# Kernel tuning notes

Hardware: AMD Instinct MI355X
Metric: run time of the kernel (lower is better)

## Reference

```python
import jax, jax.numpy as jnp
import numpy as np
import math

D_MODEL = 1024
N_HEADS = 16
D_HEAD = D_MODEL // N_HEADS


def setup_inputs() -> dict:
    key = jax.random.key(0)
    ks = jax.random.split(key, 5)
    B, T, C = 4, 2048, D_MODEL
    s = 1.0 / math.sqrt(C)
    return {
        "x": jax.random.normal(ks[0], (B, T, C), dtype=jnp.float32),
        "qkv_w": jax.random.normal(ks[1], (3 * C, C), dtype=jnp.float32) * s,
        "qkv_b": jnp.zeros((3 * C,), dtype=jnp.float32),
        "out_w": jax.random.normal(ks[2], (C, C), dtype=jnp.float32) * s,
        "out_b": jnp.zeros((C,), dtype=jnp.float32),
    }


def reference(x, qkv_w, qkv_b, out_w, out_b):
    B, T, C = x.shape
    H, Dh = N_HEADS, D_HEAD
    qkv = x @ qkv_w.T + qkv_b              # [B,T,3C] (torch Linear: x W^T + b)
    q, k, v = jnp.split(qkv, 3, axis=-1)
    # [B,T,C] -> [B,H,T,Dh]
    q = q.reshape(B, T, H, Dh).transpose(0, 2, 1, 3)
    k = k.reshape(B, T, H, Dh).transpose(0, 2, 1, 3)
    v = v.reshape(B, T, H, Dh).transpose(0, 2, 1, 3)
    att = jnp.einsum("bhqd,bhkd->bhqk", q, k) / math.sqrt(Dh)
    causal = jnp.tril(jnp.ones((T, T), dtype=bool))  # True = keep
    att = jnp.where(causal, att, -jnp.inf)
    att = jax.nn.softmax(att, axis=-1)
    y = jnp.einsum("bhqk,bhkd->bhqd", att, v)
    y = y.transpose(0, 2, 1, 3).reshape(B, T, C)
    return y @ out_w.T + out_b
```

## Files before the change

### kernel.cpp

```cpp
#include <hip/hip_runtime.h>

typedef __attribute__((ext_vector_type(4))) float f32x4;
typedef __attribute__((ext_vector_type(16))) float f32x16;
typedef __attribute__((ext_vector_type(8))) __bf16 bf16x8;
typedef __attribute__((ext_vector_type(4))) __bf16 bf16x4;
typedef __attribute__((ext_vector_type(2))) unsigned u32x2;

#define MFMA_B16(a,b,c) __builtin_amdgcn_mfma_f32_16x16x32_bf16((a),(b),(c),0,0,0)
#define MFMA32(a,b,c)  __builtin_amdgcn_mfma_f32_32x32x16_bf16((a),(b),(c),0,0,0)

static constexpr int T_LEN  = 2048;
static constexpr int C_DIM  = 1024;
static constexpr int H_NUM  = 16;
static constexpr int D_HEADc = 64;
static constexpr float Q_PRESCALE = 0.125f * 1.4426950408889634f;

__device__ __forceinline__ void async16(const void* g, void* l) {
  __builtin_amdgcn_global_load_lds(
      (const __attribute__((address_space(1))) unsigned int*)g,
      (__attribute__((address_space(3))) unsigned int*)l, 16, 0, 0);
}

__device__ __forceinline__ unsigned cvtpk(float lo, float hi) {
  unsigned r;
  asm("v_cvt_pk_bf16_f32 %0, %1, %2" : "=v"(r) : "v"(lo), "v"(hi));
  return r;
}

__global__ __launch_bounds__(256) void cvt3_kernel(const float* __restrict__ a, __bf16* __restrict__ da, int na,
                                                   const float* __restrict__ b, __bf16* __restrict__ db, int nb,
                                                   const float* __restrict__ c, __bf16* __restrict__ dc, int nc) {
  int i = blockIdx.x * 256 + threadIdx.x;
  const float* s;
  __bf16* d;
  long j;
  if (i < na) { s = a; d = da; j = i; }
  else if (i < na + nb) { s = b; d = db; j = i - na; }
  else if (i < na + nb + nc) { s = c; d = dc; j = i - na - nb; }
  else return;
  float4 f = reinterpret_cast<const float4*>(s)[j];
  bf16x4 o;
  o.x = (__bf16)f.x; o.y = (__bf16)f.y; o.z = (__bf16)f.z; o.w = (__bf16)f.w;
  reinterpret_cast<bf16x4*>(d)[j] = o;
}

__global__ __launch_bounds__(512, 2) void gemm_qkv(const __bf16* __restrict__ A,
                                                   const __bf16* __restrict__ W,
                                                   const float* __restrict__ bias,
                                                   __bf16* __restrict__ qb,
                                                   __bf16* __restrict__ kb,
                                                   __bf16* __restrict__ vb) {
  constexpr int K = 1024;
  __shared__ __bf16 As[2][128 * 64];
  __shared__ __bf16 Bs[2][128 * 64];
  const int tid = threadIdx.x;
  const int wid = tid >> 6, lane = tid & 63, l16 = lane & 15, lg = lane >> 4;
  const int r8 = lane >> 3, sl = lane & 7;
  const int r7 = l16 & 7;
  const int wm = wid >> 2, wn = wid & 3;
  const int m0 = blockIdx.x * 128;
  const int n0 = blockIdx.y * 128;

  f32x4 acc[4][2];
#pragma unroll
  for (int i = 0; i < 4; ++i)
#pragma unroll
    for (int j = 0; j < 2; ++j) acc[i][j] = f32x4{0.f, 0.f, 0.f, 0.f};

  auto stageg = [&](int buf, int k0) {
#pragma unroll
    for (int it = 0; it < 2; ++it) {
      int chunk = it * 8 + wid;
      int row = chunk * 8 + r8;
      int scol = ((sl ^ (row & 7)) << 3);
      async16(A + (long)(m0 + row) * K + k0 + scol, &As[buf][chunk * 512]);
      async16(W + (long)(n0 + row) * K + k0 + scol, &Bs[buf][chunk * 512]);
    }
  };

  stageg(0, 0);
  int cur = 0;
  for (int k0 = 0; k0 < K; k0 += 64) {
    if (k0 + 64 < K) {
      stageg(cur ^ 1, k0 + 64);
      asm volatile("s_waitcnt vmcnt(4)" ::: "memory");
    } else {
      asm volatile("s_waitcnt vmcnt(0)" ::: "memory");
    }
    __builtin_amdgcn_s_barrier();
#pragma unroll
    for (int kt = 0; kt < 2; ++kt) {
      const int sw = ((((kt << 2) | lg) ^ r7) << 3);
      bf16x8 af[4], bfv[2];
#pragma unroll
      for (int mi = 0; mi < 4; ++mi)
        af[mi] = *reinterpret_cast<const bf16x8*>(&As[cur][(wm * 64 + mi * 16 + l16) * 64 + sw]);
#pragma unroll
      for (int nt = 0; nt < 2; ++nt)
        bfv[nt] = *reinterpret_cast<const bf16x8*>(&Bs[cur][(wn * 32 + nt * 16 + l16) * 64 + sw]);
#pragma unroll
      for (int mi = 0; mi < 4; ++mi)
#pragma unroll
        for (int nt = 0; nt < 2; ++nt)
          acc[mi][nt] = MFMA_B16(af[mi], bfv[nt], acc[mi][nt]);
    }
    __builtin_amdgcn_s_barrier();
    cur ^= 1;
  }

  const int which = n0 >> 10;
  if (which == 0) {
#pragma unroll
    for (int mi = 0; mi < 4; ++mi)
#pragma unroll
      for (int nt = 0; nt < 2; ++nt)
#pragma unroll
        for (int r = 0; r < 4; ++r) {
          int m = m0 + wm * 64 + mi * 16 + lg * 4 + r;
          int n = n0 + wn * 32 + nt * 16 + l16;
          int cc = n & 1023;
          int h = cc >> 6, d = cc & 63;
          long b = m >> 11, t = m & 2047;
          qb[(((b * H_NUM + h) * T_LEN) + t) * D_HEADc + d] =
              (__bf16)((acc[mi][nt][r] + bias[n]) * Q_PRESCALE);
        }
  } else if (which == 1) {
#pragma unroll
    for (int mi = 0; mi < 4; ++mi)
#pragma unroll
      for (int nt = 0; nt < 2; ++nt)
#pragma unroll
        for (int r = 0; r < 4; ++r) {
          int m = m0 + wm * 64 + mi * 16 + lg * 4 + r;
          int n = n0 + wn * 32 + nt * 16 + l16;
          int cc = n & 1023;
          int h = cc >> 6, d = cc & 63;
          long b = m >> 11, t = m & 2047;
          kb[(((b * H_NUM + h) * T_LEN) + t) * D_HEADc + d] = (__bf16)(acc[mi][nt][r] + bias[n]);
        }
  } else {
#pragma unroll
    for (int mi = 0; mi < 4; ++mi)
#pragma unroll
      for (int nt = 0; nt < 2; ++nt) {
        int n = n0 + wn * 32 + nt * 16 + l16;
        int cc = n & 1023;
        int h = cc >> 6, d = cc & 63;
        int t0 = m0 + wm * 64 + mi * 16 + lg * 4;
        long b = t0 >> 11;
        long t = t0 & 2047;
        float bv = bias[n];
        bf16x4 pk;
#pragma unroll
        for (int r = 0; r < 4; ++r) pk[r] = (__bf16)(acc[mi][nt][r] + bv);
        *reinterpret_cast<bf16x4*>(
            &vb[(((b * H_NUM + h) * D_HEADc) + d) * T_LEN + t]) = pk;
      }
  }
}

__global__ __launch_bounds__(512, 4) void attn_kernel(const __bf16* __restrict__ q,
                                                      const __bf16* __restrict__ k,
                                                      const __bf16* __restrict__ vt,
                                                      __bf16* __restrict__ y) {
  __shared__ __bf16 Ks[2][2][64 * 64];
  __shared__ __bf16 Vs[2][2][64 * 64];
  const int tid = threadIdx.x;
  const int wid = tid >> 6, lane = tid & 63;
  const int l31 = lane & 31, hi = lane >> 5;
  const int r8 = lane >> 3, sl = lane & 7;
  const int r7 = l31 & 7;
  const int bid = blockIdx.x;
  const int qt = 15 - (bid >> 6);
  const int bh = bid & 63;
  const int grp = wid >> 2;
  const int wq = wid & 3;
  const int q0 = qt * 128;
  const int qw = q0 + wq * 32;
  const int qglob = qw + l31;
  const __bf16* qg = q + (long)bh * T_LEN * D_HEADc;
  const __bf16* kg = k + (long)bh * T_LEN * D_HEADc;
  const __bf16* vg = vt + (long)bh * T_LEN * D_HEADc;
  const long bb = bh >> 4;
  const int h = bh & 15;

  union { unsigned short us[8]; bf16x8 v; } ones_u;
#pragma unroll
  for (int i = 0; i < 8; ++i) ones_u.us[i] = 0x3F80;
  const bf16x8 ones = ones_u.v;

  f32x16 z16;
#pragma unroll
  for (int r = 0; r < 16; ++r) z16[r] = 0.f;

  bf16x8 qf[4];
#pragma unroll
  for (int dt = 0; dt < 4; ++dt)
    qf[dt] = *reinterpret_cast<const bf16x8*>(qg + (long)qglob * D_HEADc + dt * 16 + hi * 8);

  f32x16 o[2];
  o[0] = z16; o[1] = z16;
  f32x16 lacc = z16;

  auto stage = [&](int buf, int i) {
#pragma unroll
    for (int it = 0; it < 4; ++it) {
      int slot = it * 8 + wid;
      int g = slot & 7;
      int kind = slot >> 3;
      int par = kind >> 1, isv = kind & 1;
      int row = g * 8 + r8;
      int scol = ((sl ^ (row & 7)) << 3);
      int k0s = (2 * i + par) * 64;
      if (!isv)
        async16(kg + (long)(k0s + row) * D_HEADc + scol, &Ks[buf][par][g * 512]);
      else
        async16(vg + (long)row * T_LEN + k0s + scol, &Vs[buf][par][g * 512]);
    }
  };

  const int iters = qt + 1;
  stage(0, 0);
  int cur = 0;
  for (int i = 0; i < iters; ++i) {
    if (i + 1 < iters) {
      stage(cur ^ 1, i + 1);
      asm volatile("s_waitcnt vmcnt(4)" ::: "memory");
    } else {
      asm volatile("s_waitcnt vmcnt(0)" ::: "memory");
    }
    __builtin_amdgcn_s_barrier();
    const int k0 = (2 * i + grp) * 64;
    if (k0 < qw + 32) {
      const __bf16* Kc = Ks[cur][grp];
      const __bf16* Vc = Vs[cur][grp];
      f32x16 s[2];
      __builtin_amdgcn_s_setprio(1);
      {
        const int swz = (hi ^ r7) << 3;
        bf16x8 kf0 = *reinterpret_cast<const bf16x8*>(&Kc[l31 * 64 + swz]);
        bf16x8 kf1 = *reinterpret_cast<const bf16x8*>(&Kc[(32 + l31) * 64 + swz]);
        s[0] = MFMA32(kf0, qf[0], z16);
        s[1] = MFMA32(kf1, qf[0], z16);
      }
#pragma unroll
      for (int dt = 1; dt < 4; ++dt) {
        const int swz = (((dt << 1) | hi) ^ r7) << 3;
        bf16x8 kf0 = *reinterpret_cast<const bf16x8*>(&Kc[l31 * 64 + swz]);
        bf16x8 kf1 = *reinterpret_cast<const bf16x8*>(&Kc[(32 + l31) * 64 + swz]);
        s[0] = MFMA32(kf0, qf[dt], s[0]);
        s[1] = MFMA32(kf1, qf[dt], s[1]);
      }
      __builtin_amdgcn_s_setprio(0);

      if (k0 + 63 > qw) {
#pragma unroll
        for (int r = 0; r < 16; ++r) {
          const int kb = (r & 3) + 8 * (r >> 2) + 4 * hi;
          if (k0 + kb > qglob) s[0][r] = -3e38f;
          if (k0 + 32 + kb > qglob) s[1][r] = -3e38f;
        }
      }

#pragma unroll
      for (int ki = 0; ki < 2; ++ki)
#pragma unroll
        for (int r = 0; r < 16; ++r) s[ki][r] = exp2f(s[ki][r]);

      unsigned pb[4][4];
#pragma unroll
      for (int ki = 0; ki < 2; ++ki) {
        unsigned d0 = cvtpk(s[ki][0], s[ki][1]),   d1 = cvtpk(s[ki][2], s[ki][3]);
        unsigned d2 = cvtpk(s[ki][4], s[ki][5]),   d3 = cvtpk(s[ki][6], s[ki][7]);
        unsigned d4 = cvtpk(s[ki][8], s[ki][9]),   d5 = cvtpk(s[ki][10], s[ki][11]);
        unsigned d6 = cvtpk(s[ki][12], s[ki][13]), d7 = cvtpk(s[ki][14], s[ki][15]);
        u32x2 a2 = __builtin_amdgcn_permlane32_swap(d0, d2, false, false);
        u32x2 b2 = __builtin_amdgcn_permlane32_swap(d1, d3, false, false);
        pb[ki * 2][0] = a2[0]; pb[ki * 2][1] = b2[0];
        pb[ki * 2][2] = a2[1]; pb[ki * 2][3] = b2[1];
        u32x2 c2 = __builtin_amdgcn_permlane32_swap(d4, d6, false, false);
        u32x2 e2 = __builtin_amdgcn_permlane32_swap(d5, d7, false, false);
        pb[ki * 2 + 1][0] = c2[0]; pb[ki * 2 + 1][1] = e2[0];
        pb[ki * 2 + 1][2] = c2[1]; pb[ki * 2 + 1][3] = e2[1];
      }

      __builtin_amdgcn_s_setprio(1);
#pragma unroll
      for (int kt = 0; kt < 4; ++kt) {
        union { unsigned u[4]; bf16x8 v; } pu;
#pragma unroll
        for (int w = 0; w < 4; ++w) pu.u[w] = pb[kt][w];
        const int swz = (((kt << 1) | hi) ^ r7) << 3;
        bf16x8 vf0 = *reinterpret_cast<const bf16x8*>(&Vc[l31 * 64 + swz]);
        bf16x8 vf1 = *reinterpret_cast<const bf16x8*>(&Vc[(32 + l31) * 64 + swz]);
        o[0] = MFMA32(vf0, pu.v, o[0]);
        o[1] = MFMA32(vf1, pu.v, o[1]);
        lacc = MFMA32(ones, pu.v, lacc);
      }
      __builtin_amdgcn_s_setprio(0);
    }
    __builtin_amdgcn_s_barrier();
    cur ^= 1;
  }

  float* ob  = (float*)&Ks[0][0][0];
  float* lb  = (float*)&Vs[0][0][0];
  if (grp == 1) {
#pragma unroll
    for (int di = 0; di < 2; ++di)
#pragma unroll
      for (int r = 0; r < 16; ++r) {
        const int kb = (r & 3) + 8 * (r >> 2) + 4 * hi;
        ob[wq * 2048 + (di * 32 + kb) * 32 + l31] = o[di][r];
      }
    if (hi == 0) lb[wq * 32 + l31] = lacc[0];
  }
  __syncthreads();
  if (grp == 0) {
    const float inv = 1.f / (lacc[0] + lb[wq * 32 + l31]);
    const long row = bb * T_LEN + qglob;
#pragma unroll
    for (int di = 0; di < 2; ++di)
#pragma unroll
      for (int rr = 0; rr < 4; ++rr) {
        bf16x4 pk;
#pragma unroll
        for (int c = 0; c < 4; ++c) {
          const int r = rr * 4 + c;
          const int kb = rr * 8 + hi * 4 + c;
          float val = o[di][r] + ob[wq * 2048 + (di * 32 + kb) * 32 + l31];
          pk[c] = (__bf16)(val * inv);
        }
        *reinterpret_cast<bf16x4*>(
            &y[row * C_DIM + h * D_HEADc + di * 32 + rr * 8 + hi * 4]) = pk;
      }
  }
}

__global__ __launch_bounds__(512, 2) void gemm_proj(const __bf16* __restrict__ A,
                                                    const __bf16* __restrict__ W,
                                                    const float* __restrict__ bias,
                                                    float* __restrict__ out) {
  constexpr int K = 1024;
  __shared__ __bf16 As[2][128 * 64];
  __shared__ __bf16 Bs[2][128 * 64];
  const int tid = threadIdx.x;
  const int wid = tid >> 6, lane = tid & 63, l16 = lane & 15, lg = lane >> 4;
  const int r8 = lane >> 3, sl = lane & 7;
  const int r7 = l16 & 7;
  const int wm = wid >> 2, wn = wid & 3;
  const int m0 = blockIdx.x * 128, n0 = blockIdx.y * 128;

  f32x4 acc[4][2];
#pragma unroll
  for (int i = 0; i < 4; ++i)
#pragma unroll
    for (int j = 0; j < 2; ++j) acc[i][j] = f32x4{0.f, 0.f, 0.f, 0.f};

  auto stageg = [&](int buf, int k0) {
#pragma unroll
    for (int it = 0; it < 2; ++it) {
      int chunk = it * 8 + wid;
      int row = chunk * 8 + r8;
      int scol = ((sl ^ (row & 7)) << 3);
      async16(A + (long)(m0 + row) * K + k0 + scol, &As[buf][chunk * 512]);
      async16(W + (long)(n0 + row) * K + k0 + scol, &Bs[buf][chunk * 512]);
    }
  };

  stageg(0, 0);
  int cur = 0;
  for (int k0 = 0; k0 < K; k0 += 64) {
    if (k0 + 64 < K) {
      stageg(cur ^ 1, k0 + 64);
      asm volatile("s_waitcnt vmcnt(4)" ::: "memory");
    } else {
      asm volatile("s_waitcnt vmcnt(0)" ::: "memory");
    }
    __builtin_amdgcn_s_barrier();
#pragma unroll
    for (int kt = 0; kt < 2; ++kt) {
      const int sw = ((((kt << 2) | lg) ^ r7) << 3);
      bf16x8 af[4], bfv[2];
#pragma unroll
      for (int mi = 0; mi < 4; ++mi)
        af[mi] = *reinterpret_cast<const bf16x8*>(&As[cur][(wm * 64 + mi * 16 + l16) * 64 + sw]);
#pragma unroll
      for (int nt = 0; nt < 2; ++nt)
        bfv[nt] = *reinterpret_cast<const bf16x8*>(&Bs[cur][(wn * 32 + nt * 16 + l16) * 64 + sw]);
#pragma unroll
      for (int mi = 0; mi < 4; ++mi)
#pragma unroll
        for (int nt = 0; nt < 2; ++nt)
          acc[mi][nt] = MFMA_B16(af[mi], bfv[nt], acc[mi][nt]);
    }
    __builtin_amdgcn_s_barrier();
    cur ^= 1;
  }
#pragma unroll
  for (int mi = 0; mi < 4; ++mi)
#pragma unroll
    for (int nt = 0; nt < 2; ++nt)
#pragma unroll
      for (int r = 0; r < 4; ++r) {
        long m = m0 + wm * 64 + mi * 16 + lg * 4 + r;
        int n = n0 + wn * 32 + nt * 16 + l16;
        out[m * C_DIM + n] = acc[mi][nt][r] + bias[n];
      }
}

extern "C" void kernel_launch(void* const* d_in, const int* in_sizes, int n_in,
                              void* d_out, int out_size, void* d_ws, size_t ws_size,
                              hipStream_t stream) {
  const float* x     = (const float*)d_in[0];
  const float* qkv_w = (const float*)d_in[1];
  const float* qkv_b = (const float*)d_in[2];
  const float* out_w = (const float*)d_in[3];
  const float* out_b = (const float*)d_in[4];
  float* out = (float*)d_out;

  const long NX  = 8192L * 1024;
  const long NWQ = 3072L * 1024;
  const long NWO = 1024L * 1024;
  const size_t need = (size_t)(5 * NX + NWQ + NWO) * 2;
  if (ws_size < need) return;

  __bf16* xb   = (__bf16*)d_ws;
  __bf16* wqkv = xb + NX;
  __bf16* wout = wqkv + NWQ;
  __bf16* qb   = wout + NWO;
  __bf16* kb   = qb + NX;
  __bf16* vb   = kb + NX;
  __bf16* yb   = vb + NX;

  const int na = (int)(NX / 4), nb = (int)(NWQ / 4), nc = (int)(NWO / 4);
  cvt3_kernel<<<(na + nb + nc + 255) / 256, 256, 0, stream>>>(x, xb, na, qkv_w, wqkv, nb, out_w, wout, nc);

  gemm_qkv<<<dim3(64, 24), 512, 0, stream>>>(xb, wqkv, qkv_b, qb, kb, vb);
  attn_kernel<<<dim3(1024), 512, 0, stream>>>(qb, kb, vb, yb);
  gemm_proj<<<dim3(64, 8), 512, 0, stream>>>(yb, wout, out_b, out);
}
```

Baseline: 162.9 us.

## Halve attention KV tile to 32 keys and reverse q-tile order for later blocks

```diff
diff --git a/kernel.cpp b/kernel.cpp
--- a/kernel.cpp
+++ b/kernel.cpp
@@ -163,15 +163,19 @@
                                                       const __bf16* __restrict__ k,
                                                       const __bf16* __restrict__ vt,
                                                       __bf16* __restrict__ y) {
-  __shared__ __bf16 Ks[2][2][64 * 64];
-  __shared__ __bf16 Vs[2][2][64 * 64];
+  __shared__ union {
+    struct { __bf16 K[2][2][32 * 64]; __bf16 V[2][2][64 * 32]; } st;
+    float ob[8192];
+  } sm;
+  __shared__ float lbuf[128];
   const int tid = threadIdx.x;
   const int wid = tid >> 6, lane = tid & 63;
   const int l31 = lane & 31, hi = lane >> 5;
   const int r8 = lane >> 3, sl = lane & 7;
+  const int r4 = lane >> 2, sl4 = lane & 3;
   const int r7 = l31 & 7;
   const int bid = blockIdx.x;
-  const int qt = 15 - (bid >> 6);
+  const int qt = (bid < 512) ? (15 - (bid >> 6)) : ((bid - 512) >> 6);
   const int bh = bid & 63;
   const int grp = wid >> 2;
   const int wq = wid & 3;
@@ -204,95 +208,88 @@
 
   auto stage = [&](int buf, int i) {
 #pragma unroll
-    for (int it = 0; it < 4; ++it) {
+    for (int it = 0; it < 2; ++it) {
       int slot = it * 8 + wid;
-      int g = slot & 7;
-      int kind = slot >> 3;
+      int kind = slot >> 2;
       int par = kind >> 1, isv = kind & 1;
-      int row = g * 8 + r8;
-      int scol = ((sl ^ (row & 7)) << 3);
-      int k0s = (2 * i + par) * 64;
-      if (!isv)
-        async16(kg + (long)(k0s + row) * D_HEADc + scol, &Ks[buf][par][g * 512]);
-      else
-        async16(vg + (long)row * T_LEN + k0s + scol, &Vs[buf][par][g * 512]);
+      int g = slot & 3;
+      int k0s = (2 * i + par) * 32;
+      if (!isv) {
+        int row = g * 8 + r8;
+        int scol = ((sl ^ (row & 7)) << 3);
+        async16(kg + (long)(k0s + row) * D_HEADc + scol, &sm.st.K[buf][par][g * 512]);
+      } else {
+        int d = g * 16 + r4;
+        int scol = ((sl4 ^ ((d >> 1) & 3)) << 3);
+        async16(vg + (long)d * T_LEN + k0s + scol, &sm.st.V[buf][par][g * 512]);
+      }
     }
   };
 
-  const int iters = qt + 1;
+  const int iters = 2 * qt + 2;
   stage(0, 0);
   int cur = 0;
   for (int i = 0; i < iters; ++i) {
     if (i + 1 < iters) {
       stage(cur ^ 1, i + 1);
-      asm volatile("s_waitcnt vmcnt(4)" ::: "memory");
+      asm volatile("s_waitcnt vmcnt(2)" ::: "memory");
     } else {
       asm volatile("s_waitcnt vmcnt(0)" ::: "memory");
     }
     __builtin_amdgcn_s_barrier();
-    const int k0 = (2 * i + grp) * 64;
+    const int k0 = (2 * i + grp) * 32;
     if (k0 < qw + 32) {
-      const __bf16* Kc = Ks[cur][grp];
-      const __bf16* Vc = Vs[cur][grp];
-      f32x16 s[2];
+      const __bf16* Kc = sm.st.K[cur][grp];
+      const __bf16* Vc = sm.st.V[cur][grp];
+      f32x16 s;
       __builtin_amdgcn_s_setprio(1);
       {
         const int swz = (hi ^ r7) << 3;
-        bf16x8 kf0 = *reinterpret_cast<const bf16x8*>(&Kc[l31 * 64 + swz]);
-        bf16x8 kf1 = *reinterpret_cast<const bf16x8*>(&Kc[(32 + l31) * 64 + swz]);
-        s[0] = MFMA32(kf0, qf[0], z16);
-        s[1] = MFMA32(kf1, qf[0], z16);
+        bf16x8 kf = *reinterpret_cast<const bf16x8*>(&Kc[l31 * 64 + swz]);
+        s = MFMA32(kf, qf[0], z16);
       }
 #pragma unroll
       for (int dt = 1; dt < 4; ++dt) {
         const int swz = (((dt << 1) | hi) ^ r7) << 3;
-        bf16x8 kf0 = *reinterpret_cast<const bf16x8*>(&Kc[l31 * 64 + swz]);
-        bf16x8 kf1 = *reinterpret_cast<const bf16x8*>(&Kc[(32 + l31) * 64 + swz]);
-        s[0] = MFMA32(kf0, qf[dt], s[0]);
-        s[1] = MFMA32(kf1, qf[dt], s[1]);
+        bf16x8 kf = *reinterpret_cast<const bf16x8*>(&Kc[l31 * 64 + swz]);
+        s = MFMA32(kf, qf[dt], s);
       }
       __builtin_amdgcn_s_setprio(0);
 
-      if (k0 + 63 > qw) {
+      if (k0 + 31 > qw) {
 #pragma unroll
         for (int r = 0; r < 16; ++r) {
           const int kb = (r & 3) + 8 * (r >> 2) + 4 * hi;
-          if (k0 + kb > qglob) s[0][r] = -3e38f;
-          if (k0 + 32 + kb > qglob) s[1][r] = -3e38f;
+          if (k0 + kb > qglob) s[r] = -3e38f;
         }
       }
 
 #pragma unroll
-      for (int ki = 0; ki < 2; ++ki)
-#pragma unroll
-        for (int r = 0; r < 16; ++r) s[ki][r] = exp2f(s[ki][r]);
-
-      unsigned pb[4][4];
-#pragma unroll
-      for (int ki = 0; ki < 2; ++ki) {
-        unsigned d0 = cvtpk(s[ki][0], s[ki][1]),   d1 = cvtpk(s[ki][2], s[ki][3]);
-        unsigned d2 = cvtpk(s[ki][4], s[ki][5]),   d3 = cvtpk(s[ki][6], s[ki][7]);
-        unsigned d4 = cvtpk(s[ki][8], s[ki][9]),   d5 = cvtpk(s[ki][10], s[ki][11]);
-        unsigned d6 = cvtpk(s[ki][12], s[ki][13]), d7 = cvtpk(s[ki][14], s[ki][15]);
+      for (int r = 0; r < 16; ++r) s[r] = exp2f(s[r]);
+
+      unsigned pb[2][4];
+      {
+        unsigned d0 = cvtpk(s[0], s[1]),   d1 = cvtpk(s[2], s[3]);
+        unsigned d2 = cvtpk(s[4], s[5]),   d3 = cvtpk(s[6], s[7]);
+        unsigned d4 = cvtpk(s[8], s[9]),   d5 = cvtpk(s[10], s[11]);
+        unsigned d6 = cvtpk(s[12], s[13]), d7 = cvtpk(s[14], s[15]);
         u32x2 a2 = __builtin_amdgcn_permlane32_swap(d0, d2, false, false);
         u32x2 b2 = __builtin_amdgcn_permlane32_swap(d1, d3, false, false);
-        pb[ki * 2][0] = a2[0]; pb[ki * 2][1] = b2[0];
-        pb[ki * 2][2] = a2[1]; pb[ki * 2][3] = b2[1];
+        pb[0][0] = a2[0]; pb[0][1] = b2[0]; pb[0][2] = a2[1]; pb[0][3] = b2[1];
         u32x2 c2 = __builtin_amdgcn_permlane32_swap(d4, d6, false, false);
         u32x2 e2 = __builtin_amdgcn_permlane32_swap(d5, d7, false, false);
-        pb[ki * 2 + 1][0] = c2[0]; pb[ki * 2 + 1][1] = e2[0];
-        pb[ki * 2 + 1][2] = c2[1]; pb[ki * 2 + 1][3] = e2[1];
+        pb[1][0] = c2[0]; pb[1][1] = e2[0]; pb[1][2] = c2[1]; pb[1][3] = e2[1];
       }
 
       __builtin_amdgcn_s_setprio(1);
 #pragma unroll
-      for (int kt = 0; kt < 4; ++kt) {
+      for (int kt = 0; kt < 2; ++kt) {
         union { unsigned u[4]; bf16x8 v; } pu;
 #pragma unroll
         for (int w = 0; w < 4; ++w) pu.u[w] = pb[kt][w];
-        const int swz = (((kt << 1) | hi) ^ r7) << 3;
-        bf16x8 vf0 = *reinterpret_cast<const bf16x8*>(&Vc[l31 * 64 + swz]);
-        bf16x8 vf1 = *reinterpret_cast<const bf16x8*>(&Vc[(32 + l31) * 64 + swz]);
+        const int vswz = ((((kt << 1) | hi) ^ ((l31 >> 1) & 3)) << 3);
+        bf16x8 vf0 = *reinterpret_cast<const bf16x8*>(&Vc[l31 * 32 + vswz]);
+        bf16x8 vf1 = *reinterpret_cast<const bf16x8*>(&Vc[(32 + l31) * 32 + vswz]);
         o[0] = MFMA32(vf0, pu.v, o[0]);
         o[1] = MFMA32(vf1, pu.v, o[1]);
         lacc = MFMA32(ones, pu.v, lacc);
@@ -303,21 +300,19 @@
     cur ^= 1;
   }
 
-  float* ob  = (float*)&Ks[0][0][0];
-  float* lb  = (float*)&Vs[0][0][0];
   if (grp == 1) {
 #pragma unroll
     for (int di = 0; di < 2; ++di)
 #pragma unroll
       for (int r = 0; r < 16; ++r) {
         const int kb = (r & 3) + 8 * (r >> 2) + 4 * hi;
-        ob[wq * 2048 + (di * 32 + kb) * 32 + l31] = o[di][r];
-      }
-    if (hi == 0) lb[wq * 32 + l31] = lacc[0];
+        sm.ob[wq * 2048 + (di * 32 + kb) * 32 + l31] = o[di][r];
+      }
+    if (hi == 0) lbuf[wq * 32 + l31] = lacc[0];
   }
   __syncthreads();
   if (grp == 0) {
-    const float inv = 1.f / (lacc[0] + lb[wq * 32 + l31]);
+    const float inv = 1.f / (lacc[0] + lbuf[wq * 32 + l31]);
     const long row = bb * T_LEN + qglob;
 #pragma unroll
     for (int di = 0; di < 2; ++di)
@@ -328,7 +323,7 @@
         for (int c = 0; c < 4; ++c) {
           const int r = rr * 4 + c;
           const int kb = rr * 8 + hi * 4 + c;
-          float val = o[di][r] + ob[wq * 2048 + (di * 32 + kb) * 32 + l31];
+          float val = o[di][r] + sm.ob[wq * 2048 + (di * 32 + kb) * 32 + l31];
           pk[c] = (__bf16)(val * inv);
         }
         *reinterpret_cast<bf16x4*>(
```

After: 257.3 us. 1.58x slower.
